# Kernel tuning notes

Measured on AMD Instinct MI355X. Metric: run time of the kernel, lower is better.

Reference implementation:

```python
import jax, jax.numpy as jnp
import numpy as np

D_MODEL = 1024
N_EXPERTS = 8
TOP_K = 2
CAP_FACTOR = 1.0
HIDDEN = 2816  # multiple_of*ceil(int(2*4*d/3)/multiple_of) with multiple_of=256


def setup_inputs() -> dict:
    key = jax.random.key(0)
    ks = jax.random.split(key, 8)
    B, S = 2, 2048
    s = 0.02
    return {
        "x": jax.random.normal(ks[0], (B, S, D_MODEL), jnp.float32),
        "noise": jax.random.normal(ks[1], (B, S, N_EXPERTS), jnp.float32),
        "router_w": jax.random.normal(ks[2], (N_EXPERTS, D_MODEL), jnp.float32) * s,
        "router_b": jnp.zeros((N_EXPERTS,), jnp.float32),
        "noise_w": jax.random.normal(ks[3], (N_EXPERTS, D_MODEL), jnp.float32) * s,
        "noise_b": jnp.zeros((N_EXPERTS,), jnp.float32),
        "w1": jax.random.normal(ks[4], (N_EXPERTS, HIDDEN, D_MODEL), jnp.float32) * s,
        "w3": jax.random.normal(ks[5], (N_EXPERTS, HIDDEN, D_MODEL), jnp.float32) * s,
        "w2": jax.random.normal(ks[6], (N_EXPERTS, D_MODEL, HIDDEN), jnp.float32) * s,
    }


def reference(x, noise, router_w, router_b, noise_w, noise_b, w1, w3, w2):
    B, S, d = x.shape
    N = B * S
    capacity = int(N * TOP_K / N_EXPERTS * CAP_FACTOR)
    flat_x = x.reshape(N, d)

    # noisy top-k router
    logits = flat_x @ router_w.T + router_b                      # [N, E]
    noise_logits = flat_x @ noise_w.T + noise_b                  # [N, E]
    noisy = logits + noise.reshape(N, N_EXPERTS) * jax.nn.softplus(noise_logits)
    topv, topi = jax.lax.top_k(noisy, TOP_K)                     # [N, k]
    # softmax over sparse (-inf filled) logits == softmax over top-k values
    gw = jax.nn.softmax(topv, axis=-1)                           # [N, k]

    updates = jnp.zeros_like(flat_x)
    tok_ids = jnp.arange(N, dtype=jnp.int32)
    for e in range(N_EXPERTS):
        hit = topi == e                                          # [N, k]
        gate = jnp.sum(gw * hit, axis=-1)                        # [N]
        m = jnp.any(hit, axis=-1)                                # token routed to e
        pos = jnp.cumsum(m.astype(jnp.int32)) - 1                # rank in flat order
        keep = m & (pos < capacity)                              # capacity truncation (first-come)
        slot = jnp.where(keep, pos, capacity)                    # dropped tokens -> overflow slot
        # gather tokens into fixed-capacity buffer (slot `capacity` is a trash slot)
        buf = jnp.zeros((capacity + 1, d), x.dtype).at[slot].set(flat_x)
        tok = jnp.full((capacity + 1,), N, jnp.int32).at[slot].set(tok_ids)
        xb = buf[:capacity]
        # SwiGLU FFN: w2( silu(x w1^T) * (x w3^T) )
        h = jax.nn.silu(xb @ w1[e].T) * (xb @ w3[e].T)           # [cap, H]
        o = h @ w2[e].T                                          # [cap, d]
        tke = tok[:capacity]
        g = jnp.where(tke < N, gate[jnp.clip(tke, 0, N - 1)], 0.0)
        # scatter-combine; index N drops (empty slots)
        updates = updates.at[tke].add(o * g[:, None], mode="drop")
    return updates.reshape(B, S, d)
```

## Files before the change

### kernel.cpp

```cpp
#include <hip/hip_runtime.h>


#define D_MODEL 1024
#define HIDDEN 2816
#define N_TOK 4096
#define CAP 1024

typedef __attribute__((ext_vector_type(8))) short short8;
typedef __attribute__((ext_vector_type(4))) float f32x4;

__device__ __forceinline__ unsigned short f2bf(float f) {
  unsigned int u = __float_as_uint(f);
  u += 0x7fffu + ((u >> 16) & 1u);
  return (unsigned short)(u >> 16);
}
__device__ __forceinline__ float bf2f(unsigned short h) {
  return __uint_as_float(((unsigned int)h) << 16);
}

template <int Ncnt> __device__ __forceinline__ void waitv() {
  if constexpr (Ncnt == 8)      asm volatile("s_waitcnt vmcnt(8)" ::: "memory");
  else if constexpr (Ncnt == 6) asm volatile("s_waitcnt vmcnt(6)" ::: "memory");
  else                          asm volatile("s_waitcnt vmcnt(0)" ::: "memory");
}

__global__ void router_kernel(const float* __restrict__ x, const float* __restrict__ noise,
                              const float* __restrict__ rw, const float* __restrict__ rb,
                              const float* __restrict__ nw, const float* __restrict__ nb,
                              int* __restrict__ topi, float* __restrict__ gall,
                              int* __restrict__ slot) {
  int wid = threadIdx.x >> 6;
  int lane = threadIdx.x & 63;
  int t = blockIdx.x * 4 + wid;
  if (t >= N_TOK) return;
  const float* xr = x + (size_t)t * D_MODEL;
  double accL[8] = {0,0,0,0,0,0,0,0};
  double accN[8] = {0,0,0,0,0,0,0,0};
  for (int i = 0; i < 4; ++i) {
    int kb = (i * 64 + lane) * 4;
    float4 xv = *(const float4*)(xr + kb);
#pragma unroll
    for (int e = 0; e < 8; ++e) {
      float4 wv = *(const float4*)(rw + e * D_MODEL + kb);
      accL[e] += (double)xv.x * wv.x + (double)xv.y * wv.y + (double)xv.z * wv.z + (double)xv.w * wv.w;
      float4 nv = *(const float4*)(nw + e * D_MODEL + kb);
      accN[e] += (double)xv.x * nv.x + (double)xv.y * nv.y + (double)xv.z * nv.z + (double)xv.w * nv.w;
    }
  }
#pragma unroll
  for (int e = 0; e < 8; ++e) {
    for (int s = 32; s > 0; s >>= 1) {
      accL[e] += __shfl_xor(accL[e], s);
      accN[e] += __shfl_xor(accN[e], s);
    }
  }
  if (lane == 0) {
    double noisy[8];
#pragma unroll
    for (int e = 0; e < 8; ++e) {
      double lg = accL[e] + (double)rb[e];
      double nl = accN[e] + (double)nb[e];
      double sp = (nl > 0.0 ? nl : 0.0) + log1p(exp(-fabs(nl)));
      noisy[e] = lg + (double)noise[t * 8 + e] * sp;
    }
    int i0 = 0;
    for (int e = 1; e < 8; ++e) if (noisy[e] > noisy[i0]) i0 = e;
    int i1 = -1;
    for (int e = 0; e < 8; ++e) { if (e == i0) continue; if (i1 < 0 || noisy[e] > noisy[i1]) i1 = e; }
    double g0 = 1.0 / (1.0 + exp(noisy[i1] - noisy[i0]));
    topi[t * 2] = i0; topi[t * 2 + 1] = i1;
    gall[t * 2] = (float)g0; gall[t * 2 + 1] = (float)(1.0 - g0);
    slot[t * 2] = -1; slot[t * 2 + 1] = -1;
  }
}

__global__ void scan_kernel(const int* __restrict__ topi, const float* __restrict__ gall,
                            int* __restrict__ slot, int* __restrict__ tok_list,
                            float* __restrict__ gslot) {
  int e = blockIdx.x;
  int tid = threadIdx.x;
  int lane = tid & 63, wid = tid >> 6;
  __shared__ int wsum[16];
  __shared__ int base_s;
  tok_list[e * CAP + tid] = -1;
  if (tid == 0) base_s = 0;
  __syncthreads();
  for (int chunk = 0; chunk < N_TOK / 1024; ++chunk) {
    int t = chunk * 1024 + tid;
    int i0 = topi[t * 2], i1 = topi[t * 2 + 1];
    bool m = (i0 == e) || (i1 == e);
    unsigned long long mask = __ballot(m);
    int excl = __popcll(mask & ((1ull << lane) - 1ull));
    if (lane == 0) wsum[wid] = __popcll(mask);
    __syncthreads();
    int base = base_s;
    int woff = 0;
    for (int w = 0; w < wid; ++w) woff += wsum[w];
    int pos = base + woff + excl;
    if (m && pos < CAP) {
      tok_list[e * CAP + pos] = t;
      gslot[e * CAP + pos] = gall[t * 2 + (i0 == e ? 0 : 1)];
      if (i0 == e) slot[t * 2] = pos; else slot[t * 2 + 1] = pos;
    }
    __syncthreads();
    if (tid == 0) {
      int s = 0;
      for (int w = 0; w < 16; ++w) s += wsum[w];
      base_s = base + s;
    }
    __syncthreads();
  }
}

__global__ void gather_kernel(const float* __restrict__ x, const int* __restrict__ tok_list,
                              unsigned short* __restrict__ xb) {
  int row = blockIdx.x;
  int tok = tok_list[row];
  unsigned short* dst = xb + (size_t)row * D_MODEL + threadIdx.x * 4;
  if (tok < 0) {
    *(ushort4*)dst = make_ushort4(0, 0, 0, 0);
  } else {
    float4 v = *(const float4*)(x + (size_t)tok * D_MODEL + threadIdx.x * 4);
    *(ushort4*)dst = make_ushort4(f2bf(v.x), f2bf(v.y), f2bf(v.z), f2bf(v.w));
  }
}

__global__ void cvt3_kernel(const float* __restrict__ s0, const float* __restrict__ s1,
                            const float* __restrict__ s2, unsigned short* __restrict__ d0,
                            unsigned short* __restrict__ d1, unsigned short* __restrict__ d2) {
  int i = blockIdx.x * blockDim.x + threadIdx.x;
  const float* src = (blockIdx.y == 0) ? s0 : (blockIdx.y == 1) ? s1 : s2;
  unsigned short* dst = (blockIdx.y == 0) ? d0 : (blockIdx.y == 1) ? d1 : d2;
  float4 v = *(const float4*)(src + (size_t)i * 4);
  *(ushort4*)(dst + (size_t)i * 4) = make_ushort4(f2bf(v.x), f2bf(v.y), f2bf(v.z), f2bf(v.w));
}

template <int NOUT, int K, int NW, int MODE>
__global__ __launch_bounds__(512, 1)
void gemm_moe(const unsigned short* __restrict__ Ab, const unsigned short* __restrict__ B0,
              const unsigned short* __restrict__ B1, void* __restrict__ OUT,
              const int* __restrict__ tokl, const float* __restrict__ gslot) {
  constexpr int ABYTES = 32768;
  constexpr int BUFSZ = ABYTES + NW * 16384;
  constexpr int KT = K / 64;
  constexpr int SK = (MODE == 2) ? 2 : 1;
  constexpr int KTS = KT / SK;
  constexpr int BNCOL = (MODE == 2 && NW == 2) ? 256 : 128;
  constexpr int NBN = NOUT / BNCOL;
  constexpr int NWG = 8 * 4 * NBN * SK;
  constexpr int CPW = (32 + NW * 16) / 8;

  __shared__ char smem[2 * BUFSZ];

  int lid = blockIdx.x;
  int swz = (lid & 7) * (NWG / 8) + (lid >> 3);
  constexpr int PERE = 4 * NBN * SK;
  int e = swz / PERE;
  int r = swz - e * PERE;
  int bm = r / (NBN * SK);
  int r2 = r - bm * (NBN * SK);
  int bn = r2 / SK;
  int sk = r2 - bn * SK;
  int kt0 = sk * KTS;

  const unsigned short* A = Ab + (size_t)e * CAP * K;
  int tid = threadIdx.x, lane = tid & 63, wid = tid >> 6;
  int wr = wid >> 2, wc = wid & 3;
  int lane15 = lane & 15, lhi = lane >> 4, l7 = lane & 7;

  int lrow = lane >> 3;
  int lcol = ((lane & 7) ^ lrow) * 8;
  const unsigned short* Abase = A + (size_t)(bm * 256 + lrow) * K + lcol;
  const unsigned short* Bb0 = B0 + (size_t)e * NOUT * K + (size_t)(bn * BNCOL + lrow) * K + lcol;
  const unsigned short* Bb1 = (NW == 2)
      ? B1 + (size_t)e * NOUT * K + (size_t)(bn * BNCOL + lrow) * K + lcol : Bb0;

  auto STAGE = [&](int ktile, int buf) {
    char* lb = smem + buf * BUFSZ;
#pragma unroll
    for (int i = 0; i < CPW; ++i) {
      int c = wid * CPW + i;
      if (c < 32) {
        const unsigned short* g = Abase + (size_t)(c * 8) * K + ktile * 64;
        __builtin_amdgcn_global_load_lds((const __attribute__((address_space(1))) void*)g,
                                         (__attribute__((address_space(3))) void*)(lb + c * 1024), 16, 0, 0);
      } else {
        int cb2 = c - 32;
        const unsigned short* base = (cb2 >> 4) ? Bb1 : Bb0;
        const unsigned short* g = base + (size_t)((cb2 & 15) * 8) * K + ktile * 64;
        __builtin_amdgcn_global_load_lds((const __attribute__((address_space(1))) void*)g,
                                         (__attribute__((address_space(3))) void*)(lb + ABYTES + cb2 * 1024), 16, 0, 0);
      }
    }
  };

  int sw0 = ((0 + lhi) ^ l7) * 16;
  int sw1 = ((4 + lhi) ^ l7) * 16;

  f32x4 acc[8][NW][2] = {};

  STAGE(kt0, 0);
  STAGE(kt0 + 1, 1);
  waitv<CPW>();
  __builtin_amdgcn_sched_barrier(0);
  __builtin_amdgcn_s_barrier();
  __builtin_amdgcn_sched_barrier(0);

  for (int ktl = 0; ktl < KTS; ++ktl) {
    char* cb = smem + (ktl & 1) * BUFSZ;
    short8 a0[8], b0[NW][2], a1[8], b1[NW][2];
#pragma unroll
    for (int w = 0; w < NW; ++w)
#pragma unroll
      for (int n = 0; n < 2; ++n)
        b0[w][n] = *(const short8*)(cb + ABYTES + w * 16384 + wc * 4096 + n * 2048 + lane15 * 128 + sw0);
#pragma unroll
    for (int m = 0; m < 8; ++m)
      a0[m] = *(const short8*)(cb + wr * 16384 + m * 2048 + lane15 * 128 + sw0);
    __builtin_amdgcn_s_setprio(1);
#pragma unroll
    for (int m = 0; m < 8; ++m)
#pragma unroll
      for (int w = 0; w < NW; ++w)
#pragma unroll
        for (int n = 0; n < 2; ++n)
          acc[m][w][n] = __builtin_amdgcn_mfma_f32_16x16x32_bf16(a0[m], b0[w][n], acc[m][w][n], 0, 0, 0);
    __builtin_amdgcn_s_setprio(0);
#pragma unroll
    for (int w = 0; w < NW; ++w)
#pragma unroll
      for (int n = 0; n < 2; ++n)
        b1[w][n] = *(const short8*)(cb + ABYTES + w * 16384 + wc * 4096 + n * 2048 + lane15 * 128 + sw1);
#pragma unroll
    for (int m = 0; m < 8; ++m)
      a1[m] = *(const short8*)(cb + wr * 16384 + m * 2048 + lane15 * 128 + sw1);
    __builtin_amdgcn_sched_barrier(0);
    __builtin_amdgcn_s_barrier();
    __builtin_amdgcn_sched_barrier(0);
    if (ktl + 2 < KTS) STAGE(kt0 + ktl + 2, ktl & 1);
    __builtin_amdgcn_s_setprio(1);
#pragma unroll
    for (int m = 0; m < 8; ++m)
#pragma unroll
      for (int w = 0; w < NW; ++w)
#pragma unroll
        for (int n = 0; n < 2; ++n)
          acc[m][w][n] = __builtin_amdgcn_mfma_f32_16x16x32_bf16(a1[m], b1[w][n], acc[m][w][n], 0, 0, 0);
    __builtin_amdgcn_s_setprio(0);
    if (ktl + 2 < KTS) waitv<CPW>();
    else if (ktl + 1 < KTS) waitv<0>();
    __builtin_amdgcn_sched_barrier(0);
    if (ktl + 1 < KTS) __builtin_amdgcn_s_barrier();
    __builtin_amdgcn_sched_barrier(0);
  }

  if constexpr (MODE == 1) {
    unsigned short* H = (unsigned short*)OUT + (size_t)e * CAP * NOUT;
#pragma unroll
    for (int m = 0; m < 8; ++m) {
#pragma unroll
      for (int n = 0; n < 2; ++n) {
        int row0 = bm * 256 + wr * 128 + m * 16 + lhi * 4;
        int col = bn * 128 + wc * 32 + n * 16 + lane15;
#pragma unroll
        for (int j = 0; j < 4; ++j) {
          float g1 = acc[m][0][n][j];
          float g3 = acc[m][1][n][j];
          float hv = g1 / (1.0f + __expf(-g1)) * g3;
          H[(size_t)(row0 + j) * NOUT + col] = f2bf(hv);
        }
      }
    }
  } else {
    float* out = (float*)OUT;
#pragma unroll
    for (int m = 0; m < 8; ++m) {
#pragma unroll
      for (int w = 0; w < NW; ++w) {
#pragma unroll
        for (int n = 0; n < 2; ++n) {
          int row0 = bm * 256 + wr * 128 + m * 16 + lhi * 4;
          int col = bn * BNCOL + w * 128 + wc * 32 + n * 16 + lane15;
#pragma unroll
          for (int j = 0; j < 4; ++j) {
            int gr = e * CAP + row0 + j;
            int t = tokl[gr];
            if (t >= 0) {
              float g = gslot[gr];
              atomicAdd(out + (size_t)t * D_MODEL + col, g * acc[m][w][n][j]);
            }
          }
        }
      }
    }
  }
}

extern "C" void kernel_launch(void* const* d_in, const int* in_sizes, int n_in,
                              void* d_out, int out_size, void* d_ws, size_t ws_size,
                              hipStream_t stream) {
  const float* x     = (const float*)d_in[0];
  const float* noise = (const float*)d_in[1];
  const float* rw    = (const float*)d_in[2];
  const float* rb    = (const float*)d_in[3];
  const float* nw    = (const float*)d_in[4];
  const float* nb    = (const float*)d_in[5];
  const float* w1    = (const float*)d_in[6];
  const float* w3    = (const float*)d_in[7];
  const float* w2    = (const float*)d_in[8];
  float* out = (float*)d_out;

  char* ws = (char*)d_ws;
  size_t off = 0;
  auto alloc = [&](size_t bytes) -> void* {
    void* p = ws + off;
    off += (bytes + 255) & ~(size_t)255;
    return p;
  };
  const size_t WELEM = (size_t)8 * HIDDEN * D_MODEL;
  unsigned short* wb1 = (unsigned short*)alloc(WELEM * 2);
  unsigned short* wb3 = (unsigned short*)alloc(WELEM * 2);
  unsigned short* wb2 = (unsigned short*)alloc(WELEM * 2);
  unsigned short* xb  = (unsigned short*)alloc((size_t)8 * CAP * D_MODEL * 2);
  unsigned short* h   = (unsigned short*)alloc((size_t)8 * CAP * HIDDEN * 2);
  int*   topi  = (int*)alloc(N_TOK * 2 * 4);
  float* gall  = (float*)alloc(N_TOK * 2 * 4);
  int*   slot  = (int*)alloc(N_TOK * 2 * 4);
  int*   tokl  = (int*)alloc(8 * CAP * 4);
  float* gslot = (float*)alloc(8 * CAP * 4);
  (void)ws_size; (void)in_sizes; (void)n_in; (void)out_size;

  const int n4w = (int)(WELEM / 4);
  cvt3_kernel<<<dim3(n4w / 256, 3), 256, 0, stream>>>(w1, w3, w2, wb1, wb3, wb2);

  router_kernel<<<N_TOK / 4, 256, 0, stream>>>(x, noise, rw, rb, nw, nb, topi, gall, slot);
  scan_kernel<<<8, 1024, 0, stream>>>(topi, gall, slot, tokl, gslot);
  gather_kernel<<<8 * CAP, 256, 0, stream>>>(x, tokl, xb);

  hipMemsetAsync(d_out, 0, (size_t)N_TOK * D_MODEL * 4, stream);

  gemm_moe<HIDDEN, D_MODEL, 2, 1><<<dim3(704), 512, 0, stream>>>(
      xb, wb1, wb3, (void*)h, nullptr, nullptr);

  gemm_moe<D_MODEL, HIDDEN, 2, 2><<<dim3(256), 512, 0, stream>>>(
      h, wb2, wb2 + (size_t)128 * HIDDEN, (void*)out, tokl, gslot);
}
```

Baseline: 367.9 us.

## Replace atomic scatter-combine with per-split partial buffers and a gather combine kernel

```diff
diff --git a/kernel.cpp b/kernel.cpp
--- a/kernel.cpp
+++ b/kernel.cpp
@@ -74,9 +74,8 @@
   }
 }
 
-__global__ void scan_kernel(const int* __restrict__ topi, const float* __restrict__ gall,
-                            int* __restrict__ slot, int* __restrict__ tok_list,
-                            float* __restrict__ gslot) {
+__global__ void scan_kernel(const int* __restrict__ topi,
+                            int* __restrict__ slot, int* __restrict__ tok_list) {
   int e = blockIdx.x;
   int tid = threadIdx.x;
   int lane = tid & 63, wid = tid >> 6;
@@ -99,7 +98,6 @@
     int pos = base + woff + excl;
     if (m && pos < CAP) {
       tok_list[e * CAP + pos] = t;
-      gslot[e * CAP + pos] = gall[t * 2 + (i0 == e ? 0 : 1)];
       if (i0 == e) slot[t * 2] = pos; else slot[t * 2 + 1] = pos;
     }
     __syncthreads();
@@ -138,8 +136,7 @@
 template <int NOUT, int K, int NW, int MODE>
 __global__ __launch_bounds__(512, 1)
 void gemm_moe(const unsigned short* __restrict__ Ab, const unsigned short* __restrict__ B0,
-              const unsigned short* __restrict__ B1, void* __restrict__ OUT,
-              const int* __restrict__ tokl, const float* __restrict__ gslot) {
+              const unsigned short* __restrict__ B1, void* __restrict__ OUT) {
   constexpr int ABYTES = 32768;
   constexpr int BUFSZ = ABYTES + NW * 16384;
   constexpr int KT = K / 64;
@@ -272,7 +269,7 @@
       }
     }
   } else {
-    float* out = (float*)OUT;
+    float* P = (float*)OUT + (size_t)sk * 8 * CAP * NOUT + (size_t)e * CAP * NOUT;
 #pragma unroll
     for (int m = 0; m < 8; ++m) {
 #pragma unroll
@@ -282,18 +279,35 @@
           int row0 = bm * 256 + wr * 128 + m * 16 + lhi * 4;
           int col = bn * BNCOL + w * 128 + wc * 32 + n * 16 + lane15;
 #pragma unroll
-          for (int j = 0; j < 4; ++j) {
-            int gr = e * CAP + row0 + j;
-            int t = tokl[gr];
-            if (t >= 0) {
-              float g = gslot[gr];
-              atomicAdd(out + (size_t)t * D_MODEL + col, g * acc[m][w][n][j]);
-            }
-          }
+          for (int j = 0; j < 4; ++j)
+            P[(size_t)(row0 + j) * NOUT + col] = acc[m][w][n][j];
         }
       }
     }
   }
+}
+
+__global__ void combine_kernel(const float* __restrict__ ob, const int* __restrict__ topi,
+                               const float* __restrict__ gall, const int* __restrict__ slot,
+                               float* __restrict__ out) {
+  int t = blockIdx.x;
+  int d = threadIdx.x * 4;
+  const size_t HALF = (size_t)8 * CAP * D_MODEL;
+  float4 r = make_float4(0.f, 0.f, 0.f, 0.f);
+#pragma unroll
+  for (int k = 0; k < 2; ++k) {
+    int s = slot[t * 2 + k];
+    if (s >= 0) {
+      int e = topi[t * 2 + k];
+      float g = gall[t * 2 + k];
+      size_t base = ((size_t)e * CAP + s) * D_MODEL + d;
+      float4 a = *(const float4*)(ob + base);
+      float4 b = *(const float4*)(ob + HALF + base);
+      r.x += g * (a.x + b.x); r.y += g * (a.y + b.y);
+      r.z += g * (a.z + b.z); r.w += g * (a.w + b.w);
+    }
+  }
+  *(float4*)(out + (size_t)t * D_MODEL + d) = r;
 }
 
 extern "C" void kernel_launch(void* const* d_in, const int* in_sizes, int n_in,
@@ -323,25 +337,24 @@
   unsigned short* wb2 = (unsigned short*)alloc(WELEM * 2);
   unsigned short* xb  = (unsigned short*)alloc((size_t)8 * CAP * D_MODEL * 2);
   unsigned short* h   = (unsigned short*)alloc((size_t)8 * CAP * HIDDEN * 2);
+  float*          ob  = (float*)alloc((size_t)2 * 8 * CAP * D_MODEL * 4);
   int*   topi  = (int*)alloc(N_TOK * 2 * 4);
   float* gall  = (float*)alloc(N_TOK * 2 * 4);
   int*   slot  = (int*)alloc(N_TOK * 2 * 4);
   int*   tokl  = (int*)alloc(8 * CAP * 4);
-  float* gslot = (float*)alloc(8 * CAP * 4);
   (void)ws_size; (void)in_sizes; (void)n_in; (void)out_size;
 
   const int n4w = (int)(WELEM / 4);
   cvt3_kernel<<<dim3(n4w / 256, 3), 256, 0, stream>>>(w1, w3, w2, wb1, wb3, wb2);
 
   router_kernel<<<N_TOK / 4, 256, 0, stream>>>(x, noise, rw, rb, nw, nb, topi, gall, slot);
-  scan_kernel<<<8, 1024, 0, stream>>>(topi, gall, slot, tokl, gslot);
+  scan_kernel<<<8, 1024, 0, stream>>>(topi, slot, tokl);
   gather_kernel<<<8 * CAP, 256, 0, stream>>>(x, tokl, xb);
 
-  hipMemsetAsync(d_out, 0, (size_t)N_TOK * D_MODEL * 4, stream);
-
-  gemm_moe<HIDDEN, D_MODEL, 2, 1><<<dim3(704), 512, 0, stream>>>(
-      xb, wb1, wb3, (void*)h, nullptr, nullptr);
+  gemm_moe<HIDDEN, D_MODEL, 2, 1><<<dim3(704), 512, 0, stream>>>(xb, wb1, wb3, (void*)h);
 
   gemm_moe<D_MODEL, HIDDEN, 2, 2><<<dim3(256), 512, 0, stream>>>(
-      h, wb2, wb2 + (size_t)128 * HIDDEN, (void*)out, tokl, gslot);
-}
+      h, wb2, wb2 + (size_t)128 * HIDDEN, (void*)ob);
+
+  combine_kernel<<<N_TOK, 256, 0, stream>>>(ob, topi, gall, slot, out);
+}
```

After: 323.4 us. -12.1%, faster.
